# Performance work log

Hardware: AMD Instinct MI355X
Metric: run time of the kernel (lower is better)

The kernel has to match this reference:

```python
import jax, jax.numpy as jnp
import numpy as np

N_P, N_A = 200_000, 100_000
D_P, D_A, H, OUT = 64, 64, 32, 1
E_PP, E_AP, E_PA = 3_200_000, 1_600_000, 1_600_000


def _lin(key, din, dout, bias=True):
    kw, kb = jax.random.split(key)
    W = jax.random.normal(kw, (din, dout), jnp.float32) * (1.0 / np.sqrt(din))
    if bias:
        b = jax.random.normal(kb, (dout,), jnp.float32) * 0.01
        return W, b
    return W


def setup_inputs() -> dict:
    key = jax.random.key(0)
    ks = jax.random.split(key, 24)
    inp = {}
    inp['x_paper'] = jax.random.normal(ks[0], (N_P, D_P), jnp.float32)
    inp['x_author'] = jax.random.normal(ks[1], (N_A, D_A), jnp.float32)
    inp['src_pp'] = jax.random.randint(ks[2], (E_PP,), 0, N_P)
    inp['dst_pp'] = jax.random.randint(ks[3], (E_PP,), 0, N_P)
    inp['src_ap'] = jax.random.randint(ks[4], (E_AP,), 0, N_A)
    inp['dst_ap'] = jax.random.randint(ks[5], (E_AP,), 0, N_P)
    inp['src_pa'] = jax.random.randint(ks[6], (E_PA,), 0, N_P)
    inp['dst_pa'] = jax.random.randint(ks[7], (E_PA,), 0, N_A)
    # Layer-1 SAGEConv weights per relation: lin_l (neighbor, with bias), lin_r (root, no bias)
    inp['Wl1_pp'], inp['bl1_pp'] = _lin(ks[8], D_P, H)
    inp['Wr1_pp'] = _lin(ks[9], D_P, H, bias=False)
    inp['Wl1_ap'], inp['bl1_ap'] = _lin(ks[10], D_A, H)
    inp['Wr1_ap'] = _lin(ks[11], D_P, H, bias=False)
    inp['Wl1_pa'], inp['bl1_pa'] = _lin(ks[12], D_P, H)
    inp['Wr1_pa'] = _lin(ks[13], D_A, H, bias=False)
    # Layer-2 SAGEConv weights (only relations feeding 'paper' affect the output)
    inp['Wl2_pp'], inp['bl2_pp'] = _lin(ks[14], H, H)
    inp['Wr2_pp'] = _lin(ks[15], H, H, bias=False)
    inp['Wl2_ap'], inp['bl2_ap'] = _lin(ks[16], H, H)
    inp['Wr2_ap'] = _lin(ks[17], H, H, bias=False)
    # Final classifier Linear(32, 1)
    inp['W_lin'], inp['b_lin'] = _lin(ks[18], H, OUT)
    return inp


def _sage_rel(x_src, x_dst, src, dst, Wl, bl, Wr):
    # SAGEConv: lin_l(mean_{j in N(i)} x_j) + lin_r(x_i)
    n_dst = x_dst.shape[0]
    agg = jax.ops.segment_sum(x_src[src], dst, num_segments=n_dst)
    cnt = jax.ops.segment_sum(jnp.ones((src.shape[0],), x_src.dtype), dst, num_segments=n_dst)
    mean = agg / jnp.maximum(cnt, 1.0)[:, None]
    return mean @ Wl + bl + x_dst @ Wr


def reference(x_paper, x_author, src_pp, dst_pp, src_ap, dst_ap, src_pa, dst_pa,
              Wl1_pp, bl1_pp, Wr1_pp, Wl1_ap, bl1_ap, Wr1_ap, Wl1_pa, bl1_pa, Wr1_pa,
              Wl2_pp, bl2_pp, Wr2_pp, Wl2_ap, bl2_ap, Wr2_ap, W_lin, b_lin):
    # Layer 1 (to_hetero: sum per-relation conv outputs per destination type), then relu
    p1 = (_sage_rel(x_paper, x_paper, src_pp, dst_pp, Wl1_pp, bl1_pp, Wr1_pp)
          + _sage_rel(x_author, x_paper, src_ap, dst_ap, Wl1_ap, bl1_ap, Wr1_ap))
    a1 = _sage_rel(x_paper, x_author, src_pa, dst_pa, Wl1_pa, bl1_pa, Wr1_pa)
    p1, a1 = jax.nn.relu(p1), jax.nn.relu(a1)
    # Layer 2: only 'paper' output is consumed downstream
    p2 = (_sage_rel(p1, p1, src_pp, dst_pp, Wl2_pp, bl2_pp, Wr2_pp)
          + _sage_rel(a1, p1, src_ap, dst_ap, Wl2_ap, bl2_ap, Wr2_ap))
    # model_config is None -> plain Linear, no sigmoid/softmax
    return p2 @ W_lin + b_lin
```

## Files before the change

### kernel.cpp

```cpp
#include <hip/hip_runtime.h>


typedef unsigned short ushort_t;
typedef __attribute__((ext_vector_type(8))) short bf16x8;
typedef __attribute__((ext_vector_type(4))) float f32x4;

#define PWBITS 10
#define PWIN   (1 << PWBITS)
#define PCHUNK 8192
#define CAPPAD 4096

__device__ inline ushort_t f2bf(float f) {
    unsigned u = __float_as_uint(f);
    unsigned r = (u + 0x7FFFu + ((u >> 16) & 1u)) >> 16;
    return (ushort_t)r;
}
__device__ inline float bf2f_lo(unsigned u) { return __uint_as_float(u << 16); }
__device__ inline float bf2f_hi(unsigned u) { return __uint_as_float(u & 0xFFFF0000u); }
__device__ inline int ntl(const int* p) { return __builtin_nontemporal_load(p); }
__device__ inline unsigned ntlu(const unsigned* p) { return __builtin_nontemporal_load(p); }

__global__ void prep_weights(
    const float* __restrict__ Wl1_pp, const float* __restrict__ Wr1_pp,
    const float* __restrict__ Wl1_ap, const float* __restrict__ Wr1_ap,
    const float* __restrict__ Wl1_pa, const float* __restrict__ Wr1_pa,
    const float* __restrict__ bl1_pp, const float* __restrict__ bl1_ap,
    const float* __restrict__ bl1_pa,
    const float* __restrict__ Wl2_pp, const float* __restrict__ bl2_pp,
    const float* __restrict__ Wr2_pp,
    const float* __restrict__ Wl2_ap, const float* __restrict__ bl2_ap,
    const float* __restrict__ Wr2_ap,
    const float* __restrict__ W_lin, const float* __restrict__ b_lin,
    float* __restrict__ Wcomb_p,
    float* __restrict__ Wcomb_a,
    ushort_t* __restrict__ Wfrag_p,
    ushort_t* __restrict__ Wfrag_a,
    float* __restrict__ bias_p,
    float* __restrict__ bias_a,
    float* __restrict__ vv)
{
    int t = threadIdx.x;
    for (int idx = t; idx < 64 * 96; idx += 256) {
        int i = idx / 96, j = idx % 96;
        float v;
        if (j < 32)       v = Wl1_pp[i * 32 + j];
        else if (j < 64)  v = Wl1_pa[i * 32 + (j - 32)];
        else              v = Wr1_pp[i * 32 + (j - 64)] + Wr1_ap[i * 32 + (j - 64)];
        Wcomb_p[idx] = v;
    }
    for (int idx = t; idx < 64 * 64; idx += 256) {
        int i = idx / 64, j = idx % 64;
        Wcomb_a[idx] = (j < 32) ? Wl1_ap[i * 32 + j] : Wr1_pa[i * 32 + (j - 32)];
    }
    if (t < 32) {
        bias_p[t] = bl1_pp[t] + bl1_ap[t];
        bias_a[t] = bl1_pa[t];
        float vpp = 0.f, vr = 0.f, vap = 0.f;
        for (int j = 0; j < 32; ++j) {
            float wl = W_lin[j];
            vpp += Wl2_pp[t * 32 + j] * wl;
            vr  += (Wr2_pp[t * 32 + j] + Wr2_ap[t * 32 + j]) * wl;
            vap += Wl2_ap[t * 32 + j] * wl;
        }
        vv[t] = vpp; vv[32 + t] = vr; vv[96 + t] = vap;
    }
    if (t == 0) {
        float c = b_lin[0];
        for (int j = 0; j < 32; ++j) c += (bl2_pp[j] + bl2_ap[j]) * W_lin[j];
        vv[64] = c;
    }
    __syncthreads();
    for (int idx = t; idx < 12 * 64 * 8; idx += 256) {
        int f = idx >> 9, l = (idx >> 3) & 63, j = idx & 7;
        int nt = f >> 1, kh = f & 1;
        int k = kh * 32 + 8 * (l >> 4) + j;
        int n = nt * 16 + (l & 15);
        Wfrag_p[idx] = f2bf(Wcomb_p[k * 96 + n]);
    }
    for (int idx = t; idx < 8 * 64 * 8; idx += 256) {
        int f = idx >> 9, l = (idx >> 3) & 63, j = idx & 7;
        int nt = f >> 1, kh = f & 1;
        int k = kh * 32 + 8 * (l >> 4) + j;
        int n = nt * 16 + (l & 15);
        Wfrag_a[idx] = f2bf(Wcomb_a[k * 64 + n]);
    }
}

__global__ __launch_bounds__(256)
void partition3(
    const int* __restrict__ src0, const int* __restrict__ dst0, int E0,
    unsigned* __restrict__ bk0, int cap0, int nw0, int* __restrict__ wc0,
    const int* __restrict__ src1, const int* __restrict__ dst1, int E1,
    unsigned* __restrict__ bk1, int cap1, int nw1, int* __restrict__ wc1,
    const int* __restrict__ src2, const int* __restrict__ dst2, int E2,
    unsigned* __restrict__ bk2, int cap2, int nw2, int* __restrict__ wc2)
{
    __shared__ int lcnt[256];
    __shared__ int lbase[256];
    int nb0 = (E0 + PCHUNK - 1) / PCHUNK;
    int nb1 = (E1 + PCHUNK - 1) / PCHUNK;
    int b = blockIdx.x;
    const int* src; const int* dst; int E; unsigned* bk; int cap; int nw; int* wc; int chunk;
    if (b < nb0)            { src = src0; dst = dst0; E = E0; bk = bk0; cap = cap0; nw = nw0; wc = wc0; chunk = b; }
    else if (b < nb0 + nb1) { src = src1; dst = dst1; E = E1; bk = bk1; cap = cap1; nw = nw1; wc = wc1; chunk = b - nb0; }
    else                    { src = src2; dst = dst2; E = E2; bk = bk2; cap = cap2; nw = nw2; wc = wc2; chunk = b - nb0 - nb1; }
    int e0 = chunk * PCHUNK;
    int e1 = e0 + PCHUNK; if (e1 > E) e1 = E;
    for (int i = threadIdx.x; i < nw; i += 256) lcnt[i] = 0;
    __syncthreads();
    for (int e = e0 + threadIdx.x; e < e1; e += 256)
        atomicAdd(&lcnt[((unsigned)ntl(dst + e)) >> PWBITS], 1);
    __syncthreads();
    for (int i = threadIdx.x; i < nw; i += 256) {
        int c = lcnt[i];
        lbase[i] = (c > 0) ? atomicAdd(&wc[i], c) : 0;
        lcnt[i] = 0;
    }
    __syncthreads();
    for (int e = e0 + threadIdx.x; e < e1; e += 256) {
        int d = ntl(dst + e);
        int w = ((unsigned)d) >> PWBITS;
        int off = lbase[w] + atomicAdd(&lcnt[w], 1);
        if (off < cap)
            bk[(size_t)w * cap + off] =
                (((unsigned)(d & (PWIN - 1))) << 18) | (unsigned)ntl(src + e);
    }
}

__global__ __launch_bounds__(256)
void fill_win3(
    const unsigned* __restrict__ bk0, const int* __restrict__ wc0, int cap0,
    int* __restrict__ csr0, int* __restrict__ cnt0, int* __restrict__ rs0, int N0, int nw0,
    const unsigned* __restrict__ bk1, const int* __restrict__ wc1, int cap1,
    int* __restrict__ csr1, int* __restrict__ cnt1, int* __restrict__ rs1, int N1, int nw1,
    const unsigned* __restrict__ bk2, const int* __restrict__ wc2, int cap2,
    int* __restrict__ csr2, int* __restrict__ cnt2, int* __restrict__ rs2, int N2, int nw2)
{
    __shared__ int lc[PWIN];
    __shared__ int wsum[4], wpre[4];
    int b = blockIdx.x;
    const unsigned* bk; const int* wc; int cap; int* csr; int* cnt; int* rs; int N; int w;
    if (b < nw0)            { bk = bk0; wc = wc0; cap = cap0; csr = csr0; cnt = cnt0; rs = rs0; N = N0; w = b; }
    else if (b < nw0 + nw1) { bk = bk1; wc = wc1; cap = cap1; csr = csr1; cnt = cnt1; rs = rs1; N = N1; w = b - nw0; }
    else                    { bk = bk2; wc = wc2; cap = cap2; csr = csr2; cnt = cnt2; rs = rs2; N = N2; w = b - nw0 - nw1; }
    int d0 = w << PWBITS;
    int sz = wc[w]; if (sz > cap) sz = cap;
    const unsigned* bkt = bk + (size_t)w * cap;
    for (int i = threadIdx.x; i < PWIN; i += 256) lc[i] = 0;
    __syncthreads();
    for (int i = threadIdx.x; i < sz; i += 256)
        atomicAdd(&lc[ntlu(bkt + i) >> 18], 1);
    __syncthreads();
    for (int i = threadIdx.x; i < PWIN; i += 256) {
        int d = d0 + i;
        if (d < N) cnt[d] = lc[i];
    }
    __syncthreads();
    int bi = threadIdx.x * 4;
    int v[4]; int ts = 0;
#pragma unroll
    for (int k = 0; k < 4; ++k) { v[k] = lc[bi + k]; ts += v[k]; }
    int lane = threadIdx.x & 63;
    int wid = threadIdx.x >> 6;
    int incl = ts;
#pragma unroll
    for (int off = 1; off < 64; off <<= 1) {
        int o = __shfl_up(incl, off);
        if (lane >= off) incl += o;
    }
    if (lane == 63) wsum[wid] = incl;
    __syncthreads();
    if (threadIdx.x == 0) {
        int r = 0;
        for (int i = 0; i < 4; ++i) { wpre[i] = r; r += wsum[i]; }
    }
    __syncthreads();
    int run = w * cap + wpre[wid] + (incl - ts);
#pragma unroll
    for (int k = 0; k < 4; ++k) {
        int d = d0 + bi + k;
        lc[bi + k] = run;
        if (d < N) rs[d] = run;
        run += v[k];
    }
    __syncthreads();
    for (int i = threadIdx.x; i < sz; i += 256) {
        unsigned u = ntlu(bkt + i);
        int pos = atomicAdd(&lc[u >> 18], 1);
        csr[pos] = (int)(u & 0x3FFFFu);
    }
}

__device__ inline bf16x8 cvt8(const float* p) {
    float4 a = *(const float4*)p;
    float4 b = *(const float4*)(p + 4);
    bf16x8 r;
    r[0] = (short)f2bf(a.x); r[1] = (short)f2bf(a.y);
    r[2] = (short)f2bf(a.z); r[3] = (short)f2bf(a.w);
    r[4] = (short)f2bf(b.x); r[5] = (short)f2bf(b.y);
    r[6] = (short)f2bf(b.z); r[7] = (short)f2bf(b.w);
    return r;
}

__global__ __launch_bounds__(256)
void proj_paper_mfma(const float* __restrict__ x, const ushort_t* __restrict__ Wfrag,
                     const float* __restrict__ bias,
                     ushort_t* __restrict__ h_pp, ushort_t* __restrict__ h_pa,
                     float* __restrict__ root_p, int N)
{
    int wave = threadIdx.x >> 6, lane = threadIdx.x & 63;
    int mbase = blockIdx.x * 64 + wave * 16;
    int row = lane & 15, grp = lane >> 4;
    int nA = mbase + row; if (nA > N - 1) nA = N - 1;
    const float* xr = x + (size_t)nA * 64 + grp * 8;
    bf16x8 a0 = cvt8(xr);
    bf16x8 a1 = cvt8(xr + 32);
    f32x4 acc0 = {0.f, 0.f, 0.f, 0.f}, acc1 = acc0, acc2 = acc0, acc3 = acc0;
    float bp0 = bias[row];
    float bp1 = bias[16 + row];
    f32x4 acc4 = {bp0, bp0, bp0, bp0};
    f32x4 acc5 = {bp1, bp1, bp1, bp1};
    const bf16x8* wf = (const bf16x8*)(Wfrag) + lane;
    acc0 = __builtin_amdgcn_mfma_f32_16x16x32_bf16(a0, wf[0 * 64], acc0, 0, 0, 0);
    acc0 = __builtin_amdgcn_mfma_f32_16x16x32_bf16(a1, wf[1 * 64], acc0, 0, 0, 0);
    acc1 = __builtin_amdgcn_mfma_f32_16x16x32_bf16(a0, wf[2 * 64], acc1, 0, 0, 0);
    acc1 = __builtin_amdgcn_mfma_f32_16x16x32_bf16(a1, wf[3 * 64], acc1, 0, 0, 0);
    acc2 = __builtin_amdgcn_mfma_f32_16x16x32_bf16(a0, wf[4 * 64], acc2, 0, 0, 0);
    acc2 = __builtin_amdgcn_mfma_f32_16x16x32_bf16(a1, wf[5 * 64], acc2, 0, 0, 0);
    acc3 = __builtin_amdgcn_mfma_f32_16x16x32_bf16(a0, wf[6 * 64], acc3, 0, 0, 0);
    acc3 = __builtin_amdgcn_mfma_f32_16x16x32_bf16(a1, wf[7 * 64], acc3, 0, 0, 0);
    acc4 = __builtin_amdgcn_mfma_f32_16x16x32_bf16(a0, wf[8 * 64], acc4, 0, 0, 0);
    acc4 = __builtin_amdgcn_mfma_f32_16x16x32_bf16(a1, wf[9 * 64], acc4, 0, 0, 0);
    acc5 = __builtin_amdgcn_mfma_f32_16x16x32_bf16(a0, wf[10 * 64], acc5, 0, 0, 0);
    acc5 = __builtin_amdgcn_mfma_f32_16x16x32_bf16(a1, wf[11 * 64], acc5, 0, 0, 0);
    int col = row;
    int node0 = mbase + grp * 4;
#pragma unroll
    for (int reg = 0; reg < 4; ++reg) {
        int nd = node0 + reg;
        if (nd < N) {
            size_t b32 = (size_t)nd * 32;
            h_pp[b32 + col]        = f2bf(acc0[reg]);
            h_pp[b32 + 16 + col]   = f2bf(acc1[reg]);
            h_pa[b32 + col]        = f2bf(acc2[reg]);
            h_pa[b32 + 16 + col]   = f2bf(acc3[reg]);
            root_p[b32 + col]      = acc4[reg];
            root_p[b32 + 16 + col] = acc5[reg];
        }
    }
}

__global__ __launch_bounds__(256)
void proj_author_mfma(const float* __restrict__ x, const ushort_t* __restrict__ Wfrag,
                      const float* __restrict__ bias,
                      ushort_t* __restrict__ h_ap, float* __restrict__ root_a, int N)
{
    int wave = threadIdx.x >> 6, lane = threadIdx.x & 63;
    int mbase = blockIdx.x * 64 + wave * 16;
    int row = lane & 15, grp = lane >> 4;
    int nA = mbase + row; if (nA > N - 1) nA = N - 1;
    const float* xr = x + (size_t)nA * 64 + grp * 8;
    bf16x8 a0 = cvt8(xr);
    bf16x8 a1 = cvt8(xr + 32);
    f32x4 acc0 = {0.f, 0.f, 0.f, 0.f}, acc1 = acc0;
    float bp0 = bias[row];
    float bp1 = bias[16 + row];
    f32x4 acc2 = {bp0, bp0, bp0, bp0};
    f32x4 acc3 = {bp1, bp1, bp1, bp1};
    const bf16x8* wf = (const bf16x8*)(Wfrag) + lane;
    acc0 = __builtin_amdgcn_mfma_f32_16x16x32_bf16(a0, wf[0 * 64], acc0, 0, 0, 0);
    acc0 = __builtin_amdgcn_mfma_f32_16x16x32_bf16(a1, wf[1 * 64], acc0, 0, 0, 0);
    acc1 = __builtin_amdgcn_mfma_f32_16x16x32_bf16(a0, wf[2 * 64], acc1, 0, 0, 0);
    acc1 = __builtin_amdgcn_mfma_f32_16x16x32_bf16(a1, wf[3 * 64], acc1, 0, 0, 0);
    acc2 = __builtin_amdgcn_mfma_f32_16x16x32_bf16(a0, wf[4 * 64], acc2, 0, 0, 0);
    acc2 = __builtin_amdgcn_mfma_f32_16x16x32_bf16(a1, wf[5 * 64], acc2, 0, 0, 0);
    acc3 = __builtin_amdgcn_mfma_f32_16x16x32_bf16(a0, wf[6 * 64], acc3, 0, 0, 0);
    acc3 = __builtin_amdgcn_mfma_f32_16x16x32_bf16(a1, wf[7 * 64], acc3, 0, 0, 0);
    int col = row;
    int node0 = mbase + grp * 4;
#pragma unroll
    for (int reg = 0; reg < 4; ++reg) {
        int nd = node0 + reg;
        if (nd < N) {
            size_t b32 = (size_t)nd * 32;
            h_ap[b32 + col]        = f2bf(acc0[reg]);
            h_ap[b32 + 16 + col]   = f2bf(acc1[reg]);
            root_a[b32 + col]      = acc2[reg];
            root_a[b32 + 16 + col] = acc3[reg];
        }
    }
}

#define ACC8(A, U) \
    A[0] += bf2f_lo((U).x); A[1] += bf2f_hi((U).x); \
    A[2] += bf2f_lo((U).y); A[3] += bf2f_hi((U).y); \
    A[4] += bf2f_lo((U).z); A[5] += bf2f_hi((U).z); \
    A[6] += bf2f_lo((U).w); A[7] += bf2f_hi((U).w);

__global__ __launch_bounds__(256, 8)
void pull_paper(const ushort_t* __restrict__ h_pp, const ushort_t* __restrict__ h_ap,
                const float* __restrict__ root,
                const int* __restrict__ csr_pp, const int* __restrict__ rs_pp,
                const int* __restrict__ cnt_pp,
                const int* __restrict__ csr_ap, const int* __restrict__ rs_ap,
                const int* __restrict__ cnt_ap,
                const float* __restrict__ vv,
                float* __restrict__ s_pp, float* __restrict__ out, int N)
{
    __shared__ float v0[32], v1[32];
    __shared__ float c2s;
    if (threadIdx.x < 32) { v0[threadIdx.x] = vv[threadIdx.x]; v1[threadIdx.x] = vv[32 + threadIdx.x]; }
    if (threadIdx.x == 0) c2s = vv[64];
    __syncthreads();
    int n = blockIdx.x * 64 + (threadIdx.x >> 2);
    if (n >= N) return;
    int c = threadIdx.x & 3;
    float a[8];
#pragma unroll
    for (int k = 0; k < 8; ++k) a[k] = 0.f;
    int s1 = rs_pp[n], k1 = cnt_pp[n], e1 = s1 + k1;
    int j = s1;
    for (; j + 4 <= e1; j += 4) {
        int i0 = ntl(csr_pp + j), i1 = ntl(csr_pp + j + 1);
        int i2 = ntl(csr_pp + j + 2), i3 = ntl(csr_pp + j + 3);
        uint4 u0 = ((const uint4*)(h_pp + (size_t)i0 * 32))[c];
        uint4 u1 = ((const uint4*)(h_pp + (size_t)i1 * 32))[c];
        uint4 u2 = ((const uint4*)(h_pp + (size_t)i2 * 32))[c];
        uint4 u3 = ((const uint4*)(h_pp + (size_t)i3 * 32))[c];
        ACC8(a, u0) ACC8(a, u1) ACC8(a, u2) ACC8(a, u3)
    }
    for (; j < e1; ++j) {
        uint4 u0 = ((const uint4*)(h_pp + (size_t)ntl(csr_pp + j) * 32))[c];
        ACC8(a, u0)
    }
    float b[8];
#pragma unroll
    for (int k = 0; k < 8; ++k) b[k] = 0.f;
    int s2 = rs_ap[n], k2 = cnt_ap[n], e2 = s2 + k2;
    j = s2;
    for (; j + 4 <= e2; j += 4) {
        int i0 = ntl(csr_ap + j), i1 = ntl(csr_ap + j + 1);
        int i2 = ntl(csr_ap + j + 2), i3 = ntl(csr_ap + j + 3);
        uint4 u0 = ((const uint4*)(h_ap + (size_t)i0 * 32))[c];
        uint4 u1 = ((const uint4*)(h_ap + (size_t)i1 * 32))[c];
        uint4 u2 = ((const uint4*)(h_ap + (size_t)i2 * 32))[c];
        uint4 u3 = ((const uint4*)(h_ap + (size_t)i3 * 32))[c];
        ACC8(b, u0) ACC8(b, u1) ACC8(b, u2) ACC8(b, u3)
    }
    for (; j < e2; ++j) {
        uint4 u0 = ((const uint4*)(h_ap + (size_t)ntl(csr_ap + j) * 32))[c];
        ACC8(b, u0)
    }
    float ipp = 1.0f / fmaxf((float)k1, 1.0f);
    float iap = 1.0f / fmaxf((float)k2, 1.0f);
    const float* rt = root + (size_t)n * 32 + 8 * c;
    float d0 = 0.f, d1 = 0.f;
#pragma unroll
    for (int k = 0; k < 8; ++k) {
        float p = fmaxf(rt[k] + a[k] * ipp + b[k] * iap, 0.f);
        d0 += p * v0[8 * c + k];
        d1 += p * v1[8 * c + k];
    }
    d0 += __shfl_xor(d0, 1); d0 += __shfl_xor(d0, 2);
    d1 += __shfl_xor(d1, 1); d1 += __shfl_xor(d1, 2);
    if (c == 0) { s_pp[n] = d0; out[n] = d1 + c2s; }
}

__global__ __launch_bounds__(256, 8)
void pull_author(const ushort_t* __restrict__ h_pa, const float* __restrict__ root,
                 const int* __restrict__ csr_pa, const int* __restrict__ rs_pa,
                 const int* __restrict__ cnt_pa,
                 const float* __restrict__ vv, float* __restrict__ s_ap, int N)
{
    __shared__ float v0[32];
    if (threadIdx.x < 32) v0[threadIdx.x] = vv[96 + threadIdx.x];
    __syncthreads();
    int n = blockIdx.x * 64 + (threadIdx.x >> 2);
    if (n >= N) return;
    int c = threadIdx.x & 3;
    float a[8];
#pragma unroll
    for (int k = 0; k < 8; ++k) a[k] = 0.f;
    int s1 = rs_pa[n], k1 = cnt_pa[n], e1 = s1 + k1;
    int j = s1;
    for (; j + 4 <= e1; j += 4) {
        int i0 = ntl(csr_pa + j), i1 = ntl(csr_pa + j + 1);
        int i2 = ntl(csr_pa + j + 2), i3 = ntl(csr_pa + j + 3);
        uint4 u0 = ((const uint4*)(h_pa + (size_t)i0 * 32))[c];
        uint4 u1 = ((const uint4*)(h_pa + (size_t)i1 * 32))[c];
        uint4 u2 = ((const uint4*)(h_pa + (size_t)i2 * 32))[c];
        uint4 u3 = ((const uint4*)(h_pa + (size_t)i3 * 32))[c];
        ACC8(a, u0) ACC8(a, u1) ACC8(a, u2) ACC8(a, u3)
    }
    for (; j < e1; ++j) {
        uint4 u0 = ((const uint4*)(h_pa + (size_t)ntl(csr_pa + j) * 32))[c];
        ACC8(a, u0)
    }
    float ip = 1.0f / fmaxf((float)k1, 1.0f);
    const float* rt = root + (size_t)n * 32 + 8 * c;
    float d0 = 0.f;
#pragma unroll
    for (int k = 0; k < 8; ++k) {
        float p = fmaxf(rt[k] + a[k] * ip, 0.f);
        d0 += p * v0[8 * c + k];
    }
    d0 += __shfl_xor(d0, 1); d0 += __shfl_xor(d0, 2);
    if (c == 0) s_ap[n] = d0;
}

__global__ __launch_bounds__(256, 8)
void pull2(const float* __restrict__ s_pp, const float* __restrict__ s_ap,
           const int* __restrict__ csr_pp, const int* __restrict__ rs_pp,
           const int* __restrict__ cnt_pp,
           const int* __restrict__ csr_ap, const int* __restrict__ rs_ap,
           const int* __restrict__ cnt_ap,
           float* __restrict__ out, int N)
{
    int g = (blockIdx.x * blockDim.x + threadIdx.x) >> 2;
    int c = threadIdx.x & 3;
    if (g >= N) return;
    int s1 = rs_pp[g], k1 = cnt_pp[g], e1 = s1 + k1;
    float t = 0.f;
    for (int j = s1 + c; j < e1; j += 4) t += s_pp[ntl(csr_pp + j)];
    int s2 = rs_ap[g], k2 = cnt_ap[g], e2 = s2 + k2;
    float u = 0.f;
    for (int j = s2 + c; j < e2; j += 4) u += s_ap[ntl(csr_ap + j)];
    t += __shfl_xor(t, 1); t += __shfl_xor(t, 2);
    u += __shfl_xor(u, 1); u += __shfl_xor(u, 2);
    if (c == 0) {
        out[g] += t / fmaxf((float)k1, 1.f) + u / fmaxf((float)k2, 1.f);
    }
}

extern "C" void kernel_launch(void* const* d_in, const int* in_sizes, int n_in,
                              void* d_out, int out_size, void* d_ws, size_t ws_size,
                              hipStream_t stream)
{
    const float* x_paper  = (const float*)d_in[0];
    const float* x_author = (const float*)d_in[1];
    const int* src_pp = (const int*)d_in[2];
    const int* dst_pp = (const int*)d_in[3];
    const int* src_ap = (const int*)d_in[4];
    const int* dst_ap = (const int*)d_in[5];
    const int* src_pa = (const int*)d_in[6];
    const int* dst_pa = (const int*)d_in[7];
    const float* Wl1_pp = (const float*)d_in[8];
    const float* bl1_pp = (const float*)d_in[9];
    const float* Wr1_pp = (const float*)d_in[10];
    const float* Wl1_ap = (const float*)d_in[11];
    const float* bl1_ap = (const float*)d_in[12];
    const float* Wr1_ap = (const float*)d_in[13];
    const float* Wl1_pa = (const float*)d_in[14];
    const float* bl1_pa = (const float*)d_in[15];
    const float* Wr1_pa = (const float*)d_in[16];
    const float* Wl2_pp = (const float*)d_in[17];
    const float* bl2_pp = (const float*)d_in[18];
    const float* Wr2_pp = (const float*)d_in[19];
    const float* Wl2_ap = (const float*)d_in[20];
    const float* bl2_ap = (const float*)d_in[21];
    const float* Wr2_ap = (const float*)d_in[22];
    const float* W_lin  = (const float*)d_in[23];
    const float* b_lin  = (const float*)d_in[24];

    const int NP = in_sizes[0] / 64;
    const int NA = in_sizes[1] / 64;
    const int E_PP = in_sizes[2];
    const int E_AP = in_sizes[4];
    const int E_PA = in_sizes[6];

    const int nw_pp = (NP + PWIN - 1) >> PWBITS;
    const int nw_ap = nw_pp;
    const int nw_pa = (NA + PWIN - 1) >> PWBITS;
    const int cap_pp = E_PP / nw_pp + CAPPAD;
    const int cap_ap = E_AP / nw_ap + CAPPAD;
    const int cap_pa = E_PA / nw_pa + CAPPAD;

    char* wp = (char*)d_ws;
    int* wcur = (int*)wp;             wp += 768 * 4;
    unsigned* bk_pp = (unsigned*)wp;  wp += (size_t)nw_pp * cap_pp * 4;
    unsigned* bk_ap = (unsigned*)wp;  wp += (size_t)nw_ap * cap_ap * 4;
    unsigned* bk_pa = (unsigned*)wp;  wp += (size_t)nw_pa * cap_pa * 4;
    int* csr_pp = (int*)wp;           wp += (size_t)nw_pp * cap_pp * 4;
    int* csr_ap = (int*)wp;           wp += (size_t)nw_ap * cap_ap * 4;
    int* csr_pa = (int*)wp;           wp += (size_t)nw_pa * cap_pa * 4;
    int* cnt    = (int*)wp;           wp += (size_t)(2 * NP + NA) * 4;
    int* rs     = (int*)wp;           wp += (size_t)(2 * NP + NA) * 4;
    ushort_t* h_pp = (ushort_t*)wp;   wp += (size_t)NP * 32 * 2;
    ushort_t* h_pa = (ushort_t*)wp;   wp += (size_t)NP * 32 * 2;
    ushort_t* h_ap = (ushort_t*)wp;   wp += (size_t)NA * 32 * 2;
    float* root_a = (float*)wp;       wp += (size_t)NA * 32 * 4;
    float* s_pp   = (float*)wp;       wp += (size_t)NP * 4;
    float* s_ap   = (float*)wp;       wp += (size_t)NA * 4;
    float* Wcomb_p = (float*)wp;      wp += 64 * 96 * 4;
    float* Wcomb_a = (float*)wp;      wp += 64 * 64 * 4;
    ushort_t* Wfrag_p = (ushort_t*)wp; wp += 12 * 64 * 8 * 2;
    ushort_t* Wfrag_a = (ushort_t*)wp; wp += 8 * 64 * 8 * 2;
    float* bias_p = (float*)wp;       wp += 32 * 4;
    float* bias_a = (float*)wp;       wp += 32 * 4;
    float* vv     = (float*)wp;       wp += 128 * 4;
    float* root_p = (float*)bk_pp;

    int* cnt_pp = cnt,  * cnt_ap = cnt + NP,  * cnt_pa = cnt + 2 * NP;
    int* rs_pp  = rs,   * rs_ap  = rs + NP,   * rs_pa  = rs + 2 * NP;

    float* out = (float*)d_out;

    hipMemsetAsync(wcur, 0, 768 * sizeof(int), stream);

    prep_weights<<<1, 256, 0, stream>>>(
        Wl1_pp, Wr1_pp, Wl1_ap, Wr1_ap, Wl1_pa, Wr1_pa,
        bl1_pp, bl1_ap, bl1_pa,
        Wl2_pp, bl2_pp, Wr2_pp, Wl2_ap, bl2_ap, Wr2_ap,
        W_lin, b_lin, Wcomb_p, Wcomb_a, Wfrag_p, Wfrag_a, bias_p, bias_a, vv);

    int nb_total = (E_PP + PCHUNK - 1) / PCHUNK + (E_AP + PCHUNK - 1) / PCHUNK
                 + (E_PA + PCHUNK - 1) / PCHUNK;
    partition3<<<nb_total, 256, 0, stream>>>(
        src_pp, dst_pp, E_PP, bk_pp, cap_pp, nw_pp, wcur + 0,
        src_ap, dst_ap, E_AP, bk_ap, cap_ap, nw_ap, wcur + 256,
        src_pa, dst_pa, E_PA, bk_pa, cap_pa, nw_pa, wcur + 512);

    fill_win3<<<nw_pp + nw_ap + nw_pa, 256, 0, stream>>>(
        bk_pp, wcur + 0,   cap_pp, csr_pp, cnt_pp, rs_pp, NP, nw_pp,
        bk_ap, wcur + 256, cap_ap, csr_ap, cnt_ap, rs_ap, NP, nw_ap,
        bk_pa, wcur + 512, cap_pa, csr_pa, cnt_pa, rs_pa, NA, nw_pa);

    proj_paper_mfma<<<(NP + 63) / 64, 256, 0, stream>>>(
        x_paper, Wfrag_p, bias_p, h_pp, h_pa, root_p, NP);
    proj_author_mfma<<<(NA + 63) / 64, 256, 0, stream>>>(
        x_author, Wfrag_a, bias_a, h_ap, root_a, NA);

    pull_paper<<<(NP + 63) / 64, 256, 0, stream>>>(
        h_pp, h_ap, root_p, csr_pp, rs_pp, cnt_pp, csr_ap, rs_ap, cnt_ap,
        vv, s_pp, out, NP);
    pull_author<<<(NA + 63) / 64, 256, 0, stream>>>(
        h_pa, root_a, csr_pa, rs_pa, cnt_pa, vv, s_ap, NA);

    pull2<<<((size_t)NP * 4 + 255) / 256, 256, 0, stream>>>(
        s_pp, s_ap, csr_pp, rs_pp, cnt_pp, csr_ap, rs_ap, cnt_ap, out, NP);
}
```

Baseline: 417.9 us.

## Stage partition and bucket-fill edges in registers with vector loads and smaller windows

The partition and fill_win3 kernels now load their edge chunks once into registers with int4/uint4 vector loads, then reuse those values for both the counting pass and the scatter pass. Before, each pass re-read global memory with scalar loads. Destination windows shrink from 1024 to 512 nodes, and chunks from 8192 to 4096 edges, giving more blocks and smaller LDS histograms. The per-window global counters are padded 16 ints apart to avoid atomic contention on shared cache lines. In exchange there is much higher register pressure (FW_R=12 uint4 per thread), and correctness now depends on every bucket fitting within 12288 entries.

```diff
diff --git a/kernel.cpp b/kernel.cpp
--- a/kernel.cpp
+++ b/kernel.cpp
@@ -5,10 +5,11 @@
 typedef __attribute__((ext_vector_type(8))) short bf16x8;
 typedef __attribute__((ext_vector_type(4))) float f32x4;
 
-#define PWBITS 10
+#define PWBITS 9
 #define PWIN   (1 << PWBITS)
-#define PCHUNK 8192
-#define CAPPAD 4096
+#define PCHUNK 4096
+#define CAPPAD 2048
+#define FW_R   12
 
 __device__ inline ushort_t f2bf(float f) {
     unsigned u = __float_as_uint(f);
@@ -18,7 +19,6 @@
 __device__ inline float bf2f_lo(unsigned u) { return __uint_as_float(u << 16); }
 __device__ inline float bf2f_hi(unsigned u) { return __uint_as_float(u & 0xFFFF0000u); }
 __device__ inline int ntl(const int* p) { return __builtin_nontemporal_load(p); }
-__device__ inline unsigned ntlu(const unsigned* p) { return __builtin_nontemporal_load(p); }
 
 __global__ void prep_weights(
     const float* __restrict__ Wl1_pp, const float* __restrict__ Wr1_pp,
@@ -95,8 +95,8 @@
     const int* __restrict__ src2, const int* __restrict__ dst2, int E2,
     unsigned* __restrict__ bk2, int cap2, int nw2, int* __restrict__ wc2)
 {
-    __shared__ int lcnt[256];
-    __shared__ int lbase[256];
+    __shared__ int lcnt[PWIN];
+    __shared__ int lbase[PWIN];
     int nb0 = (E0 + PCHUNK - 1) / PCHUNK;
     int nb1 = (E1 + PCHUNK - 1) / PCHUNK;
     int b = blockIdx.x;
@@ -105,25 +105,46 @@
     else if (b < nb0 + nb1) { src = src1; dst = dst1; E = E1; bk = bk1; cap = cap1; nw = nw1; wc = wc1; chunk = b - nb0; }
     else                    { src = src2; dst = dst2; E = E2; bk = bk2; cap = cap2; nw = nw2; wc = wc2; chunk = b - nb0 - nb1; }
     int e0 = chunk * PCHUNK;
-    int e1 = e0 + PCHUNK; if (e1 > E) e1 = E;
+    int d_[16], s_[16];
+#pragma unroll
+    for (int r = 0; r < 4; ++r) {
+        int base = e0 + r * 1024 + threadIdx.x * 4;
+        if (base + 3 < E) {
+            int4 dv = *(const int4*)(dst + base);
+            int4 sv = *(const int4*)(src + base);
+            d_[r * 4 + 0] = dv.x; d_[r * 4 + 1] = dv.y; d_[r * 4 + 2] = dv.z; d_[r * 4 + 3] = dv.w;
+            s_[r * 4 + 0] = sv.x; s_[r * 4 + 1] = sv.y; s_[r * 4 + 2] = sv.z; s_[r * 4 + 3] = sv.w;
+        } else {
+#pragma unroll
+            for (int k = 0; k < 4; ++k) {
+                int e = base + k;
+                d_[r * 4 + k] = (e < E) ? dst[e] : -1;
+                s_[r * 4 + k] = 0;
+            }
+        }
+    }
     for (int i = threadIdx.x; i < nw; i += 256) lcnt[i] = 0;
     __syncthreads();
-    for (int e = e0 + threadIdx.x; e < e1; e += 256)
-        atomicAdd(&lcnt[((unsigned)ntl(dst + e)) >> PWBITS], 1);
+#pragma unroll
+    for (int k = 0; k < 16; ++k)
+        if (d_[k] >= 0) atomicAdd(&lcnt[((unsigned)d_[k]) >> PWBITS], 1);
     __syncthreads();
     for (int i = threadIdx.x; i < nw; i += 256) {
         int c = lcnt[i];
-        lbase[i] = (c > 0) ? atomicAdd(&wc[i], c) : 0;
+        lbase[i] = (c > 0) ? atomicAdd(&wc[i * 16], c) : 0;
         lcnt[i] = 0;
     }
     __syncthreads();
-    for (int e = e0 + threadIdx.x; e < e1; e += 256) {
-        int d = ntl(dst + e);
-        int w = ((unsigned)d) >> PWBITS;
-        int off = lbase[w] + atomicAdd(&lcnt[w], 1);
-        if (off < cap)
-            bk[(size_t)w * cap + off] =
-                (((unsigned)(d & (PWIN - 1))) << 18) | (unsigned)ntl(src + e);
+#pragma unroll
+    for (int k = 0; k < 16; ++k) {
+        int d = d_[k];
+        if (d >= 0) {
+            int w = ((unsigned)d) >> PWBITS;
+            int off = lbase[w] + atomicAdd(&lcnt[w], 1);
+            if (off < cap)
+                bk[(size_t)w * cap + off] =
+                    (((unsigned)(d & (PWIN - 1))) << 18) | (unsigned)s_[k];
+        }
     }
 }
 
@@ -144,22 +165,40 @@
     else if (b < nw0 + nw1) { bk = bk1; wc = wc1; cap = cap1; csr = csr1; cnt = cnt1; rs = rs1; N = N1; w = b - nw0; }
     else                    { bk = bk2; wc = wc2; cap = cap2; csr = csr2; cnt = cnt2; rs = rs2; N = N2; w = b - nw0 - nw1; }
     int d0 = w << PWBITS;
-    int sz = wc[w]; if (sz > cap) sz = cap;
+    int sz = wc[w * 16]; if (sz > cap) sz = cap;
     const unsigned* bkt = bk + (size_t)w * cap;
+    uint4 u[FW_R];
+#pragma unroll
+    for (int r = 0; r < FW_R; ++r) {
+        int i4 = r * 1024 + threadIdx.x * 4;
+        if (i4 + 3 < sz) {
+            u[r] = *(const uint4*)(bkt + i4);
+        } else {
+            u[r].x = (i4 + 0 < sz) ? bkt[i4 + 0] : 0xFFFFFFFFu;
+            u[r].y = (i4 + 1 < sz) ? bkt[i4 + 1] : 0xFFFFFFFFu;
+            u[r].z = (i4 + 2 < sz) ? bkt[i4 + 2] : 0xFFFFFFFFu;
+            u[r].w = (i4 + 3 < sz) ? bkt[i4 + 3] : 0xFFFFFFFFu;
+        }
+    }
     for (int i = threadIdx.x; i < PWIN; i += 256) lc[i] = 0;
     __syncthreads();
-    for (int i = threadIdx.x; i < sz; i += 256)
-        atomicAdd(&lc[ntlu(bkt + i) >> 18], 1);
-    __syncthreads();
-    for (int i = threadIdx.x; i < PWIN; i += 256) {
+#pragma unroll
+    for (int r = 0; r < FW_R; ++r) {
+        if (u[r].x != 0xFFFFFFFFu) atomicAdd(&lc[u[r].x >> 18], 1);
+        if (u[r].y != 0xFFFFFFFFu) atomicAdd(&lc[u[r].y >> 18], 1);
+        if (u[r].z != 0xFFFFFFFFu) atomicAdd(&lc[u[r].z >> 18], 1);
+        if (u[r].w != 0xFFFFFFFFu) atomicAdd(&lc[u[r].w >> 18], 1);
+    }
+    __syncthreads();
+    {
+        int i = threadIdx.x * 2;
         int d = d0 + i;
-        if (d < N) cnt[d] = lc[i];
-    }
-    __syncthreads();
-    int bi = threadIdx.x * 4;
-    int v[4]; int ts = 0;
-#pragma unroll
-    for (int k = 0; k < 4; ++k) { v[k] = lc[bi + k]; ts += v[k]; }
+        if (d < N)     cnt[d] = lc[i];
+        if (d + 1 < N) cnt[d + 1] = lc[i + 1];
+    }
+    int t2 = threadIdx.x * 2;
+    int v0 = lc[t2], v1 = lc[t2 + 1];
+    int ts = v0 + v1;
     int lane = threadIdx.x & 63;
     int wid = threadIdx.x >> 6;
     int incl = ts;
@@ -176,18 +215,18 @@
     }
     __syncthreads();
     int run = w * cap + wpre[wid] + (incl - ts);
-#pragma unroll
-    for (int k = 0; k < 4; ++k) {
-        int d = d0 + bi + k;
-        lc[bi + k] = run;
-        if (d < N) rs[d] = run;
-        run += v[k];
-    }
-    __syncthreads();
-    for (int i = threadIdx.x; i < sz; i += 256) {
-        unsigned u = ntlu(bkt + i);
-        int pos = atomicAdd(&lc[u >> 18], 1);
-        csr[pos] = (int)(u & 0x3FFFFu);
+    lc[t2] = run;
+    if (d0 + t2 < N) rs[d0 + t2] = run;
+    run += v0;
+    lc[t2 + 1] = run;
+    if (d0 + t2 + 1 < N) rs[d0 + t2 + 1] = run;
+    __syncthreads();
+#pragma unroll
+    for (int r = 0; r < FW_R; ++r) {
+        if (u[r].x != 0xFFFFFFFFu) { int p = atomicAdd(&lc[u[r].x >> 18], 1); csr[p] = (int)(u[r].x & 0x3FFFFu); }
+        if (u[r].y != 0xFFFFFFFFu) { int p = atomicAdd(&lc[u[r].y >> 18], 1); csr[p] = (int)(u[r].y & 0x3FFFFu); }
+        if (u[r].z != 0xFFFFFFFFu) { int p = atomicAdd(&lc[u[r].z >> 18], 1); csr[p] = (int)(u[r].z & 0x3FFFFu); }
+        if (u[r].w != 0xFFFFFFFFu) { int p = atomicAdd(&lc[u[r].w >> 18], 1); csr[p] = (int)(u[r].w & 0x3FFFFu); }
     }
 }
 
@@ -471,12 +510,12 @@
     const int nw_pp = (NP + PWIN - 1) >> PWBITS;
     const int nw_ap = nw_pp;
     const int nw_pa = (NA + PWIN - 1) >> PWBITS;
-    const int cap_pp = E_PP / nw_pp + CAPPAD;
-    const int cap_ap = E_AP / nw_ap + CAPPAD;
-    const int cap_pa = E_PA / nw_pa + CAPPAD;
+    const int cap_pp = ((E_PP / nw_pp + CAPPAD) + 3) & ~3;
+    const int cap_ap = ((E_AP / nw_ap + CAPPAD) + 3) & ~3;
+    const int cap_pa = ((E_PA / nw_pa + CAPPAD) + 3) & ~3;
 
     char* wp = (char*)d_ws;
-    int* wcur = (int*)wp;             wp += 768 * 4;
+    int* wcur = (int*)wp;             wp += (size_t)3 * PWIN * 16 * 4;
     unsigned* bk_pp = (unsigned*)wp;  wp += (size_t)nw_pp * cap_pp * 4;
     unsigned* bk_ap = (unsigned*)wp;  wp += (size_t)nw_ap * cap_ap * 4;
     unsigned* bk_pa = (unsigned*)wp;  wp += (size_t)nw_pa * cap_pa * 4;
@@ -505,7 +544,7 @@
 
     float* out = (float*)d_out;
 
-    hipMemsetAsync(wcur, 0, 768 * sizeof(int), stream);
+    hipMemsetAsync(wcur, 0, (size_t)3 * PWIN * 16 * 4, stream);
 
     prep_weights<<<1, 256, 0, stream>>>(
         Wl1_pp, Wr1_pp, Wl1_ap, Wr1_ap, Wl1_pa, Wr1_pa,
@@ -517,13 +556,13 @@
                  + (E_PA + PCHUNK - 1) / PCHUNK;
     partition3<<<nb_total, 256, 0, stream>>>(
         src_pp, dst_pp, E_PP, bk_pp, cap_pp, nw_pp, wcur + 0,
-        src_ap, dst_ap, E_AP, bk_ap, cap_ap, nw_ap, wcur + 256,
-        src_pa, dst_pa, E_PA, bk_pa, cap_pa, nw_pa, wcur + 512);
+        src_ap, dst_ap, E_AP, bk_ap, cap_ap, nw_ap, wcur + PWIN * 16,
+        src_pa, dst_pa, E_PA, bk_pa, cap_pa, nw_pa, wcur + 2 * PWIN * 16);
 
     fill_win3<<<nw_pp + nw_ap + nw_pa, 256, 0, stream>>>(
-        bk_pp, wcur + 0,   cap_pp, csr_pp, cnt_pp, rs_pp, NP, nw_pp,
-        bk_ap, wcur + 256, cap_ap, csr_ap, cnt_ap, rs_ap, NP, nw_ap,
-        bk_pa, wcur + 512, cap_pa, csr_pa, cnt_pa, rs_pa, NA, nw_pa);
+        bk_pp, wcur + 0,            cap_pp, csr_pp, cnt_pp, rs_pp, NP, nw_pp,
+        bk_ap, wcur + PWIN * 16,    cap_ap, csr_ap, cnt_ap, rs_ap, NP, nw_ap,
+        bk_pa, wcur + 2 * PWIN * 16, cap_pa, csr_pa, cnt_pa, rs_pa, NA, nw_pa);
 
     proj_paper_mfma<<<(NP + 63) / 64, 256, 0, stream>>>(
         x_paper, Wfrag_p, bias_p, h_pp, h_pa, root_p, NP);
```

Result: faster. 375.6 us (-10.1%).
